# Kernel optimization log

Measured on AMD Instinct MI355X. Metric: run time of the kernel, lower is better.

## Reference

```python
import jax, jax.numpy as jnp
import numpy as np

NUM_HEADS = 8
NUM_GROUPS = 32
EPS = 1e-5


def group_norm(x, scale, bias):
    # x: (b, c, t)
    b, c, t = x.shape
    xg = x.reshape(b, NUM_GROUPS, c // NUM_GROUPS, t)
    mean = xg.mean(axis=(2, 3), keepdims=True)
    var = xg.var(axis=(2, 3), keepdims=True)
    xn = ((xg - mean) * jax.lax.rsqrt(var + EPS)).reshape(b, c, t)
    return xn * scale[None, :, None] + bias[None, :, None]


def setup_inputs() -> dict:
    key = jax.random.key(0)
    ks = jax.random.split(key, 3)
    b, c, h, w = 16, 512, 32, 32
    x = jax.random.normal(ks[0], (b, c, h, w), dtype=jnp.float32)
    gn_scale = jnp.ones((c,), jnp.float32)
    gn_bias = jnp.zeros((c,), jnp.float32)
    w_qkv = jax.random.normal(ks[1], (3 * c, c), jnp.float32) * (c ** -0.5)
    b_qkv = jnp.zeros((3 * c,), jnp.float32)
    w_proj = jax.random.normal(ks[2], (c, c), jnp.float32) * (c ** -0.5)
    b_proj = jnp.zeros((c,), jnp.float32)
    return {"x": x, "gn_scale": gn_scale, "gn_bias": gn_bias,
            "w_qkv": w_qkv, "b_qkv": b_qkv, "w_proj": w_proj, "b_proj": b_proj}


def reference(x, gn_scale, gn_bias, w_qkv, b_qkv, w_proj, b_proj):
    b, c, h, w = x.shape
    t = h * w
    xf = x.reshape(b, c, t)
    xn = group_norm(xf, gn_scale, gn_bias)
    # 1x1 conv1d == channel matmul: (b, 3c, t)
    qkv = jnp.einsum('oc,bct->bot', w_qkv, xn) + b_qkv[None, :, None]
    dh = c // NUM_HEADS
    qkv = qkv.reshape(b * NUM_HEADS, 3 * dh, t)
    q, k, v = jnp.split(qkv, 3, axis=1)  # each (b*H, dh, t)
    scale = dh ** -0.25
    logits = jnp.einsum('bct,bcs->bts', q * scale, k * scale)
    weight = jax.nn.softmax(logits.astype(jnp.float32), axis=-1).astype(logits.dtype)
    attn = jnp.einsum('bts,bcs->bct', weight, v)  # (b*H, dh, t)
    attn = attn.reshape(b, c, t)
    out = jnp.einsum('oc,bct->bot', w_proj, attn) + b_proj[None, :, None]
    return (xf + out).reshape(b, c, h, w)
```

## Files before the change

### kernel.cpp

```cpp
#include <hip/hip_runtime.h>
#include <hip/hip_bf16.h>

typedef __hip_bfloat16 bf16;
typedef __attribute__((ext_vector_type(8))) short short8;
typedef __attribute__((ext_vector_type(4))) short short4v;
typedef __attribute__((ext_vector_type(4))) float float4v;
typedef __attribute__((ext_vector_type(16))) float f32x16;
typedef __attribute__((ext_vector_type(4))) int int4v;

__device__ __forceinline__ float b2f(bf16 v) { return __bfloat162float(v); }
__device__ __forceinline__ bf16  f2b(float v) { return __float2bfloat16(v); }
__device__ __forceinline__ short f2s(float v) { bf16 h = f2b(v); return *reinterpret_cast<short*>(&h); }
__device__ __forceinline__ float s2f(short s) { bf16 h; *reinterpret_cast<short*>(&h) = s; return b2f(h); }
__device__ __forceinline__ short8 ld8(const bf16* p) { return *(const short8*)p; }

__device__ __forceinline__ float ldin(const void* p, size_t i, int f32) {
  return f32 ? ((const float*)p)[i] : b2f(((const bf16*)p)[i]);
}

__device__ __forceinline__ float4v mfma16(short8 a, short8 b, float4v c) {
  return __builtin_amdgcn_mfma_f32_16x16x32_bf16(a, b, c, 0, 0, 0);
}
__device__ __forceinline__ f32x16 mfma32(short8 a, short8 b, f32x16 c) {
  return __builtin_amdgcn_mfma_f32_32x32x16_bf16(a, b, c, 0, 0, 0);
}
__device__ __forceinline__ int cvtpk(float a, float b) {
  int r; asm("v_cvt_pk_bf16_f32 %0, %1, %2" : "=v"(r) : "v"(a), "v"(b)); return r;
}
__device__ __forceinline__ void plswap(int& x, int& y) {
  asm("v_permlane32_swap_b32 %0, %1" : "+v"(x), "+v"(y));
}

__device__ __forceinline__ void gload16(const void* g, void* l) {
  __builtin_amdgcn_global_load_lds((__attribute__((address_space(1))) void*)(void*)g,
                                   (__attribute__((address_space(3))) void*)l, 16, 0, 0);
}

#define K2SCALE 0.18033688011112042f
#define TSTRIDE 72

__global__ __launch_bounds__(256) void detect_kernel(const unsigned short* __restrict__ x,
                                                     int* __restrict__ flag) {
  __shared__ int h;
  if (threadIdx.x == 0) h = 0;
  __syncthreads();
  int local = 0;
  for (int i = threadIdx.x; i < 8192; i += 256)
    if ((x[i] & 0x7F80u) == 0x7F80u) local = 1;
  if (local) atomicOr(&h, 1);
  __syncthreads();
  if (threadIdx.x == 0) *flag = h;
}

__global__ __launch_bounds__(256) void conv2_kernel(const void* __restrict__ s1, bf16* __restrict__ d1,
                                                    const void* __restrict__ s2, bf16* __restrict__ d2,
                                                    const void* __restrict__ s3, bf16* __restrict__ d3,
                                                    const void* __restrict__ s4, bf16* __restrict__ d4,
                                                    const int* __restrict__ flagp) {
  const int f32 = *flagp;
  const int blk = blockIdx.x;
  const void* src; bf16* dst; int base, n;
  if (blk < 768)       { src = s1; dst = d1; base = blk;        n = 786432; }
  else if (blk < 1024) { src = s2; dst = d2; base = blk - 768;  n = 262144; }
  else if (blk < 1026) { src = s3; dst = d3; base = blk - 1024; n = 1536;   }
  else                 { src = s4; dst = d4; base = 0;          n = 512;    }
  int i0 = (base * 256 + threadIdx.x) * 4;
#pragma unroll
  for (int j = 0; j < 4; j++) {
    int i = i0 + j;
    if (i < n) dst[i] = f2b(ldin(src, i, f32));
  }
}

__global__ __launch_bounds__(256) void gn_stats_kernel(const void* __restrict__ x,
                                                       float2* __restrict__ stats,
                                                       const int* __restrict__ flagp) {
  const int f32 = *flagp;
  const int bg = blockIdx.x;
  const int GSZ = 16 * 1024;
  const size_t base = (size_t)bg * GSZ;
  const int tid = threadIdx.x;

  float s = 0.f, ss = 0.f;
  if (f32) {
    const float4v* xp = (const float4v*)((const float*)x + base) + tid;
#pragma unroll
    for (int i = 0; i < 16; i++) {
      float4v v = xp[i * 256];
#pragma unroll
      for (int j = 0; j < 4; j++) { s += v[j]; ss += v[j] * v[j]; }
    }
  } else {
    const short8* xp = (const short8*)((const bf16*)x + base) + tid;
#pragma unroll
    for (int i = 0; i < 8; i++) {
      short8 v = xp[i * 256];
#pragma unroll
      for (int j = 0; j < 8; j++) { float f = s2f(v[j]); s += f; ss += f * f; }
    }
  }
  for (int off = 32; off > 0; off >>= 1) {
    s  += __shfl_down(s, off);
    ss += __shfl_down(ss, off);
  }
  __shared__ float rs[4], rss[4];
  const int wave = tid >> 6, lane = tid & 63;
  if (lane == 0) { rs[wave] = s; rss[wave] = ss; }
  __syncthreads();
  if (tid == 0) {
    s  = rs[0] + rs[1] + rs[2] + rs[3];
    ss = rss[0] + rss[1] + rss[2] + rss[3];
    const float mean = s * (1.f / GSZ);
    const float var  = ss * (1.f / GSZ) - mean * mean;
    stats[bg] = make_float2(mean, rsqrtf(var + 1e-5f));
  }
}

__global__ __launch_bounds__(256) void gn_apply_kernel(const void* __restrict__ x,
                                                       const void* __restrict__ gsc,
                                                       const void* __restrict__ gbi,
                                                       const float2* __restrict__ stats,
                                                       bf16* __restrict__ xn,
                                                       const int* __restrict__ flagp) {
  const int f32 = *flagp;
  const int b = blockIdx.y;
  const int t0 = blockIdx.x * 64;
  const int cs = blockIdx.z * 128;
  const int tid = threadIdx.x;

  __shared__ float Aa[128], Bb[128];
  __shared__ short T[64][130];

  if (tid < 128) {
    const int c = cs + tid;
    const float2 st = stats[b * 32 + (c >> 4)];
    const float sc = ldin(gsc, c, f32), bi = ldin(gbi, c, f32);
    Aa[tid] = st.y * sc;
    Bb[tid] = bi - st.x * st.y * sc;
  }
  __syncthreads();

  const int row = tid >> 4;
  const int t4 = (tid & 15) * 4;
  if (f32) {
    const float* xb = (const float*)x + ((size_t)(b * 512 + cs)) * 1024 + t0 + t4;
#pragma unroll
    for (int st = 0; st < 8; st++) {
      const int c = row + st * 16;
      const float4v v = *(const float4v*)(xb + (size_t)c * 1024);
      const float aa = Aa[c], bb = Bb[c];
#pragma unroll
      for (int j = 0; j < 4; j++) T[t4 + j][c] = f2s(v[j] * aa + bb);
    }
  } else {
    const bf16* xb = (const bf16*)x + ((size_t)(b * 512 + cs)) * 1024 + t0 + t4;
#pragma unroll
    for (int st = 0; st < 8; st++) {
      const int c = row + st * 16;
      const short4v v = *(const short4v*)(xb + (size_t)c * 1024);
      const float aa = Aa[c], bb = Bb[c];
#pragma unroll
      for (int j = 0; j < 4; j++) T[t4 + j][c] = f2s(s2f(v[j]) * aa + bb);
    }
  }
  __syncthreads();

  const int cc = (tid & 63) * 2, tr = tid >> 6;
#pragma unroll
  for (int i = 0; i < 16; i++) {
    const int t2 = tr + i * 4;
    const int v = *(const int*)&T[t2][cc];
    *(int*)&xn[((size_t)(b * 1024 + t0 + t2)) * 512 + cs + cc] = v;
  }
}

__global__ __launch_bounds__(256) void qkv_kernel(const bf16* __restrict__ Wb,
                                                  const bf16* __restrict__ biasb,
                                                  const bf16* __restrict__ xn,
                                                  bf16* __restrict__ Qt,
                                                  bf16* __restrict__ Kt,
                                                  bf16* __restrict__ Vb) {
  const int bat = blockIdx.z;
  const int M0 = blockIdx.y * 128;
  const int N0 = blockIdx.x * 128;
  __shared__ short smem[18432];

  const int tid = threadIdx.x;
  const int w = tid >> 6, lane = tid & 63;
  const int col = lane & 15, g = lane >> 4;
  const int wm = (w & 1) * 64, wn = (w >> 1) * 64;

  float4v acc[4][4];
#pragma unroll
  for (int i = 0; i < 4; i++)
#pragma unroll
    for (int j = 0; j < 4; j++) acc[i][j] = (float4v)(0.f);

  int srco[2], dstb[2];
#pragma unroll
  for (int i = 0; i < 2; i++) {
    const int Gb = i * 256 + w * 64;
    dstb[i] = Gb * 8;
    const int G = Gb + lane;
    srco[i] = (G >> 2) * 512 + (G & 3) * 8;
  }
  const bf16* Ab  = Wb + (size_t)M0 * 512;
  const bf16* Bb2 = xn + ((size_t)bat * 1024 + N0) * 512;

#pragma unroll
  for (int i = 0; i < 2; i++) {
    gload16(Ab + srco[i],  &smem[dstb[i]]);
    gload16(Bb2 + srco[i], &smem[4096 + dstb[i]]);
  }
  __syncthreads();

  for (int it = 0; it < 16; ++it) {
    const int pb = it & 1;
    if (it < 15) {
      const int kn = it * 32 + 32;
      const int nb = (1 - pb) * 8192;
#pragma unroll
      for (int i = 0; i < 2; i++) {
        gload16(Ab + kn + srco[i],  &smem[nb + dstb[i]]);
        gload16(Bb2 + kn + srco[i], &smem[nb + 4096 + dstb[i]]);
      }
    }
    const short* Ap = &smem[pb * 8192];
    const short* Bp = Ap + 4096;
    short8 af[4], bf4[4];
#pragma unroll
    for (int mt = 0; mt < 4; mt++) af[mt] = *(const short8*)&Ap[(wm + mt * 16 + col) * 32 + g * 8];
#pragma unroll
    for (int nt = 0; nt < 4; nt++) bf4[nt] = *(const short8*)&Bp[(wn + nt * 16 + col) * 32 + g * 8];
#pragma unroll
    for (int mt = 0; mt < 4; mt++)
#pragma unroll
      for (int nt = 0; nt < 4; nt++) acc[mt][nt] = mfma16(af[mt], bf4[nt], acc[mt][nt]);
    __syncthreads();
  }

  const int sec = (M0 + wm) >> 6;
  const int h = sec / 3, kind = sec % 3;
  const size_t bh = (size_t)bat * 8 + h;
  const float qs = (kind == 0) ? K2SCALE : 1.f;
  short* Tw = smem + w * 4608;

  float bv[4][4];
#pragma unroll
  for (int mt = 0; mt < 4; mt++)
#pragma unroll
    for (int r = 0; r < 4; r++) bv[mt][r] = b2f(biasb[M0 + wm + mt * 16 + g * 4 + r]);

  if (kind == 2) {
#pragma unroll
    for (int mt = 0; mt < 4; mt++)
#pragma unroll
      for (int nt = 0; nt < 4; nt++)
#pragma unroll
        for (int r = 0; r < 4; r++) {
          const int lo = mt * 16 + g * 4 + r;
          const int lt = nt * 16 + col;
          Tw[lo * TSTRIDE + lt] = f2s(acc[mt][nt][r] + bv[mt][r]);
        }
#pragma unroll
    for (int j = 0; j < 8; j++) {
      const int lo = j * 8 + (lane >> 3);
      const int gr = lane & 7;
      short8 v = *(const short8*)&Tw[lo * TSTRIDE + gr * 8];
      *(short8*)(Vb + (bh * 64 + lo) * 1024 + N0 + wn + gr * 8) = v;
    }
  } else {
#pragma unroll
    for (int mt = 0; mt < 4; mt++)
#pragma unroll
      for (int nt = 0; nt < 4; nt++) {
        short4v pk;
#pragma unroll
        for (int r = 0; r < 4; r++) pk[r] = f2s((acc[mt][nt][r] + bv[mt][r]) * qs);
        *(short4v*)&Tw[(nt * 16 + col) * TSTRIDE + mt * 16 + g * 4] = pk;
      }
    bf16* dst = (kind == 0) ? Qt : Kt;
#pragma unroll
    for (int j = 0; j < 8; j++) {
      const int tl = j * 8 + (lane >> 3), c8 = (lane & 7) * 8;
      short8 v = *(const short8*)&Tw[tl * TSTRIDE + c8];
      *(short8*)(dst + (bh * 1024 + N0 + wn + tl) * 64 + c8) = v;
    }
  }
}

__global__ __launch_bounds__(256, 2) void attn_kernel(const bf16* __restrict__ Qt,
                                                      const bf16* __restrict__ Kt,
                                                      const bf16* __restrict__ Vb,
                                                      bf16* __restrict__ xattn) {
  const int bh = blockIdx.x;
  const int t0 = blockIdx.y * 256;
  const int b = bh >> 3, h = bh & 7;
  const int tid = threadIdx.x;
  const int w = tid >> 6, lane = tid & 63;
  const int qv = lane & 31, hh = lane >> 5;
  const int q0 = t0 + w * 64;

  __shared__ short Ks[8192];
  __shared__ short Vs[8192];

  const bf16* kbase = Kt + (size_t)bh * 65536;
  const bf16* vbase = Vb + (size_t)bh * 65536;

  int ksrc[2], vsrc[2];
  const int ldst0 = w * 1024, ldst1 = w * 1024 + 512;
#pragma unroll
  for (int i = 0; i < 2; i++) {
    const int G = w * 128 + i * 64 + lane;
    const int a = G >> 8, ks = (G >> 6) & 3, qvs = (G >> 1) & 31, hhs = G & 1;
    const int co = (ks * 2 + hhs) * 8;
    ksrc[i] = (a * 32 + qvs) * 64 + co;
    vsrc[i] = (a * 32 + qvs) * 1024 + co;
  }
  const int rb = (qv * 2 + hh) * 8;

  short8 qb[2][4];
#pragma unroll
  for (int qt = 0; qt < 2; qt++)
#pragma unroll
    for (int ks = 0; ks < 4; ks++)
      qb[qt][ks] = ld8(Qt + ((size_t)bh * 1024 + q0 + qt * 32 + qv) * 64 + ks * 16 + hh * 8);

  f32x16 O[2][2];
#pragma unroll
  for (int qt = 0; qt < 2; qt++)
#pragma unroll
    for (int o = 0; o < 2; o++) O[qt][o] = (f32x16)(0.f);
  float l[2] = {0.f, 0.f};
  short8 pa[2][4];

  gload16(kbase + ksrc[0], &Ks[ldst0]);
  gload16(kbase + ksrc[1], &Ks[ldst1]);
  gload16(vbase + vsrc[0], &Vs[ldst0]);
  gload16(vbase + vsrc[1], &Vs[ldst1]);
  __syncthreads();

#define SMAX(S, qt, a)                                                          \
  {                                                                             \
    _Pragma("unroll")                                                           \
    for (int j = 0; j < 16; j++) S[j] = __builtin_amdgcn_exp2f(S[j]);           \
    l[qt] += (((S[0] + S[1]) + (S[2] + S[3])) + ((S[4] + S[5]) + (S[6] + S[7])))\
       + (((S[8] + S[9]) + (S[10] + S[11])) + ((S[12] + S[13]) + (S[14] + S[15]))); \
    _Pragma("unroll")                                                           \
    for (int kp = 0; kp < 2; kp++) {                                            \
      int X  = cvtpk(S[8 * kp + 0], S[8 * kp + 1]);                             \
      int Y  = cvtpk(S[8 * kp + 4], S[8 * kp + 5]);                             \
      int X2 = cvtpk(S[8 * kp + 2], S[8 * kp + 3]);                             \
      int Y2 = cvtpk(S[8 * kp + 6], S[8 * kp + 7]);                             \
      plswap(X, Y);                                                             \
      plswap(X2, Y2);                                                           \
      const int4v wv = {X, X2, Y, Y2};                                          \
      pa[qt][(a) * 2 + kp] = __builtin_bit_cast(short8, wv);                    \
    }                                                                           \
  }

#pragma unroll 2
  for (int it = 0; it < 16; ++it) {
    const int cur = (it & 1) * 4096;
    const int nxt = 4096 - cur;
    if (it < 15) {
      gload16(kbase + (it + 1) * 4096 + ksrc[0], &Ks[nxt + ldst0]);
      gload16(kbase + (it + 1) * 4096 + ksrc[1], &Ks[nxt + ldst1]);
      gload16(vbase + (it + 1) * 64 + vsrc[0],   &Vs[nxt + ldst0]);
      gload16(vbase + (it + 1) * 64 + vsrc[1],   &Vs[nxt + ldst1]);
    }
#pragma unroll
    for (int a = 0; a < 2; a++) {
      short8 kf[4];
#pragma unroll
      for (int ks = 0; ks < 4; ks++)
        kf[ks] = *(const short8*)&Ks[cur + (a * 4 + ks) * 512 + rb];
#pragma unroll
      for (int qt = 0; qt < 2; qt++) {
        f32x16 S = (f32x16)(0.f);
#pragma unroll
        for (int ks = 0; ks < 4; ks++) S = mfma32(kf[ks], qb[qt][ks], S);
        SMAX(S, qt, a);
      }
    }
#pragma unroll
    for (int o = 0; o < 2; o++) {
      short8 vf[4];
#pragma unroll
      for (int ks = 0; ks < 4; ks++)
        vf[ks] = *(const short8*)&Vs[cur + (o * 4 + ks) * 512 + rb];
#pragma unroll
      for (int qt = 0; qt < 2; qt++)
#pragma unroll
        for (int ks = 0; ks < 4; ks++)
          O[qt][o] = mfma32(pa[qt][ks], vf[ks], O[qt][o]);
    }
    __syncthreads();
  }
#undef SMAX

#pragma unroll
  for (int qt = 0; qt < 2; qt++) {
    float lt = l[qt] + __shfl_xor(l[qt], 32);
    const float inv = 1.f / lt;
    float* lf = (float*)Ks + w * 64 + qt * 32;
    lf[qv] = inv;

    bf16* ob = xattn + ((size_t)b * 1024 + q0 + qt * 32 + 4 * hh) * 512 + h * 64 + qv;
#pragma unroll
    for (int r = 0; r < 16; r++) {
      const int qoff = (r & 3) + 8 * (r >> 2);
      const float iv = lf[qoff + 4 * hh];
      ob[(size_t)qoff * 512]      = f2b(O[qt][0][r] * iv);
      ob[(size_t)qoff * 512 + 32] = f2b(O[qt][1][r] * iv);
    }
  }
}

__global__ __launch_bounds__(256) void proj_kernel(const bf16* __restrict__ Wp,
                                                   const bf16* __restrict__ biasb,
                                                   const bf16* __restrict__ xattn,
                                                   const void* __restrict__ res,
                                                   void* __restrict__ out,
                                                   const int* __restrict__ flagp) {
  const int f32 = *flagp;
  const int bat = blockIdx.z;
  const int M0 = blockIdx.y * 128;
  const int N0 = blockIdx.x * 128;
  __shared__ short smem[18432];

  const int tid = threadIdx.x;
  const int w = tid >> 6, lane = tid & 63;
  const int col = lane & 15, g = lane >> 4;
  const int wm = (w & 1) * 64, wn = (w >> 1) * 64;

  float4v acc[4][4];
#pragma unroll
  for (int i = 0; i < 4; i++)
#pragma unroll
    for (int j = 0; j < 4; j++) acc[i][j] = (float4v)(0.f);

  int srco[2], dstb[2];
#pragma unroll
  for (int i = 0; i < 2; i++) {
    const int Gb = i * 256 + w * 64;
    dstb[i] = Gb * 8;
    const int G = Gb + lane;
    srco[i] = (G >> 2) * 512 + (G & 3) * 8;
  }
  const bf16* Ab  = Wp + (size_t)M0 * 512;
  const bf16* Bb2 = xattn + ((size_t)bat * 1024 + N0) * 512;

#pragma unroll
  for (int i = 0; i < 2; i++) {
    gload16(Ab + srco[i],  &smem[dstb[i]]);
    gload16(Bb2 + srco[i], &smem[4096 + dstb[i]]);
  }
  __syncthreads();

  for (int it = 0; it < 16; ++it) {
    const int pb = it & 1;
    if (it < 15) {
      const int kn = it * 32 + 32;
      const int nb = (1 - pb) * 8192;
#pragma unroll
      for (int i = 0; i < 2; i++) {
        gload16(Ab + kn + srco[i],  &smem[nb + dstb[i]]);
        gload16(Bb2 + kn + srco[i], &smem[nb + 4096 + dstb[i]]);
      }
    }
    const short* Ap = &smem[pb * 8192];
    const short* Bp = Ap + 4096;
    short8 af[4], bf4[4];
#pragma unroll
    for (int mt = 0; mt < 4; mt++) af[mt] = *(const short8*)&Ap[(wm + mt * 16 + col) * 32 + g * 8];
#pragma unroll
    for (int nt = 0; nt < 4; nt++) bf4[nt] = *(const short8*)&Bp[(wn + nt * 16 + col) * 32 + g * 8];
#pragma unroll
    for (int mt = 0; mt < 4; mt++)
#pragma unroll
      for (int nt = 0; nt < 4; nt++) acc[mt][nt] = mfma16(af[mt], bf4[nt], acc[mt][nt]);
    __syncthreads();
  }

  short* Tw = smem + w * 4608;
  float bv[4][4];
#pragma unroll
  for (int mt = 0; mt < 4; mt++)
#pragma unroll
    for (int r = 0; r < 4; r++) bv[mt][r] = b2f(biasb[M0 + wm + mt * 16 + g * 4 + r]);

#pragma unroll
  for (int mt = 0; mt < 4; mt++)
#pragma unroll
    for (int nt = 0; nt < 4; nt++)
#pragma unroll
      for (int r = 0; r < 4; r++) {
        const int lo = mt * 16 + g * 4 + r;
        const int lt = nt * 16 + col;
        Tw[lo * TSTRIDE + lt] = f2s(acc[mt][nt][r] + bv[mt][r]);
      }
#pragma unroll
  for (int j = 0; j < 8; j++) {
    const int lo = j * 8 + (lane >> 3);
    const int gr = lane & 7;
    short8 v = *(const short8*)&Tw[lo * TSTRIDE + gr * 8];
    const int o = M0 + wm + lo;
    const size_t ci = ((size_t)bat * 512 + o) * 1024 + N0 + wn + gr * 8;
    if (f32) {
      float4v o0, o1;
#pragma unroll
      for (int e = 0; e < 4; e++) o0[e] = s2f(v[e]) + ((const float*)res)[ci + e];
#pragma unroll
      for (int e = 0; e < 4; e++) o1[e] = s2f(v[e + 4]) + ((const float*)res)[ci + 4 + e];
      *(float4v*)((float*)out + ci) = o0;
      *(float4v*)((float*)out + ci + 4) = o1;
    } else {
      short8 ov;
#pragma unroll
      for (int e = 0; e < 8; e++)
        ov[e] = f2s(s2f(v[e]) + b2f(((const bf16*)res)[ci + e]));
      *(short8*)((bf16*)out + ci) = ov;
    }
  }
}

extern "C" void kernel_launch(void* const* d_in, const int* in_sizes, int n_in,
                              void* d_out, int out_size, void* d_ws, size_t ws_size,
                              hipStream_t stream) {
  const void* x      = d_in[0];
  const void* gsc    = d_in[1];
  const void* gbi    = d_in[2];
  const void* w_qkv  = d_in[3];
  const void* b_qkv  = d_in[4];
  const void* w_proj = d_in[5];
  const void* b_proj = d_in[6];

  char* p = (char*)d_ws;
  int*    flag  = (int*)p;                 p += 256;
  float2* stats = (float2*)p;              p += 512 * sizeof(float2);
  bf16*   xn    = (bf16*)p;                p += (size_t)16 * 1024 * 512 * 2;
  bf16*   Qt    = (bf16*)p;                p += (size_t)128 * 1024 * 64 * 2;
  bf16*   Kt    = (bf16*)p;                p += (size_t)128 * 1024 * 64 * 2;
  bf16*   Vb    = (bf16*)p;                p += (size_t)128 * 64 * 1024 * 2;
  bf16*   Wqb   = (bf16*)p;                p += (size_t)1536 * 512 * 2;
  bf16*   Wpb   = (bf16*)p;                p += (size_t)512 * 512 * 2;
  bf16*   Bqb   = (bf16*)p;                p += (size_t)1536 * 2;
  bf16*   Bpb   = (bf16*)p;                p += (size_t)512 * 2;
  bf16*   xattn = (bf16*)p;

  detect_kernel<<<1, 256, 0, stream>>>((const unsigned short*)x, flag);
  conv2_kernel<<<1027, 256, 0, stream>>>(w_qkv, Wqb, w_proj, Wpb,
                                         b_qkv, Bqb, b_proj, Bpb, flag);
  gn_stats_kernel<<<512, 256, 0, stream>>>(x, stats, flag);
  gn_apply_kernel<<<dim3(16, 16, 4), 256, 0, stream>>>(x, gsc, gbi, stats, xn, flag);
  qkv_kernel<<<dim3(8, 12, 16), 256, 0, stream>>>(Wqb, Bqb, xn, Qt, Kt, Vb);
  attn_kernel<<<dim3(128, 4), 256, 0, stream>>>(Qt, Kt, Vb, xattn);
  proj_kernel<<<dim3(8, 4, 16), 256, 0, stream>>>(Wpb, Bpb, xattn, x, d_out, flag);
}
```

Measured before the change: 206.2 us.

## Merge weight conversion with GN stats; double attention KV tile and add MFMA priority

The weight/bias bf16 conversion and group-norm statistics kernels are merged into one launch, removing a kernel boundary. The attention kernel now stages 128-key K/V tiles per iteration instead of 64, halving loop iterations and barriers. It also wraps MFMA sequences in s_setprio to favour matrix issue. The larger tiles double LDS use to 64KB per block and raise register pressure from the bigger P fragment array, which may reduce occupancy.

```diff
diff --git a/kernel.cpp b/kernel.cpp
--- a/kernel.cpp
+++ b/kernel.cpp
@@ -52,34 +52,36 @@
   if (threadIdx.x == 0) *flag = h;
 }
 
-__global__ __launch_bounds__(256) void conv2_kernel(const void* __restrict__ s1, bf16* __restrict__ d1,
-                                                    const void* __restrict__ s2, bf16* __restrict__ d2,
-                                                    const void* __restrict__ s3, bf16* __restrict__ d3,
-                                                    const void* __restrict__ s4, bf16* __restrict__ d4,
-                                                    const int* __restrict__ flagp) {
+__global__ __launch_bounds__(256) void pre_kernel(const void* __restrict__ s1, bf16* __restrict__ d1,
+                                                  const void* __restrict__ s2, bf16* __restrict__ d2,
+                                                  const void* __restrict__ s3, bf16* __restrict__ d3,
+                                                  const void* __restrict__ s4, bf16* __restrict__ d4,
+                                                  const void* __restrict__ x,
+                                                  float2* __restrict__ stats,
+                                                  const int* __restrict__ flagp) {
   const int f32 = *flagp;
   const int blk = blockIdx.x;
-  const void* src; bf16* dst; int base, n;
-  if (blk < 768)       { src = s1; dst = d1; base = blk;        n = 786432; }
-  else if (blk < 1024) { src = s2; dst = d2; base = blk - 768;  n = 262144; }
-  else if (blk < 1026) { src = s3; dst = d3; base = blk - 1024; n = 1536;   }
-  else                 { src = s4; dst = d4; base = 0;          n = 512;    }
-  int i0 = (base * 256 + threadIdx.x) * 4;
-#pragma unroll
-  for (int j = 0; j < 4; j++) {
-    int i = i0 + j;
-    if (i < n) dst[i] = f2b(ldin(src, i, f32));
-  }
-}
-
-__global__ __launch_bounds__(256) void gn_stats_kernel(const void* __restrict__ x,
-                                                       float2* __restrict__ stats,
-                                                       const int* __restrict__ flagp) {
-  const int f32 = *flagp;
-  const int bg = blockIdx.x;
+  const int tid = threadIdx.x;
+  __shared__ float rs[4], rss[4];
+
+  if (blk < 1027) {
+    const void* src; bf16* dst; int base, n;
+    if (blk < 768)       { src = s1; dst = d1; base = blk;        n = 786432; }
+    else if (blk < 1024) { src = s2; dst = d2; base = blk - 768;  n = 262144; }
+    else if (blk < 1026) { src = s3; dst = d3; base = blk - 1024; n = 1536;   }
+    else                 { src = s4; dst = d4; base = 0;          n = 512;    }
+    int i0 = (base * 256 + tid) * 4;
+#pragma unroll
+    for (int j = 0; j < 4; j++) {
+      int i = i0 + j;
+      if (i < n) dst[i] = f2b(ldin(src, i, f32));
+    }
+    return;
+  }
+
+  const int bg = blk - 1027;
   const int GSZ = 16 * 1024;
   const size_t base = (size_t)bg * GSZ;
-  const int tid = threadIdx.x;
 
   float s = 0.f, ss = 0.f;
   if (f32) {
@@ -103,7 +105,6 @@
     s  += __shfl_down(s, off);
     ss += __shfl_down(ss, off);
   }
-  __shared__ float rs[4], rss[4];
   const int wave = tid >> 6, lane = tid & 63;
   if (lane == 0) { rs[wave] = s; rss[wave] = ss; }
   __syncthreads();
@@ -301,21 +302,22 @@
   const int qv = lane & 31, hh = lane >> 5;
   const int q0 = t0 + w * 64;
 
-  __shared__ short Ks[8192];
-  __shared__ short Vs[8192];
+  __shared__ short Ks[16384];
+  __shared__ short Vs[16384];
 
   const bf16* kbase = Kt + (size_t)bh * 65536;
   const bf16* vbase = Vb + (size_t)bh * 65536;
 
-  int ksrc[2], vsrc[2];
-  const int ldst0 = w * 1024, ldst1 = w * 1024 + 512;
-#pragma unroll
-  for (int i = 0; i < 2; i++) {
-    const int G = w * 128 + i * 64 + lane;
-    const int a = G >> 8, ks = (G >> 6) & 3, qvs = (G >> 1) & 31, hhs = G & 1;
-    const int co = (ks * 2 + hhs) * 8;
-    ksrc[i] = (a * 32 + qvs) * 64 + co;
-    vsrc[i] = (a * 32 + qvs) * 1024 + co;
+  int ksrc[4], vsrc[4];
+  const int ldw = w * 2048;
+#pragma unroll
+  for (int i = 0; i < 4; i++) {
+    const int G = w * 256 + i * 64 + lane;
+    const int qvs = (G >> 1) & 31, hhs = G & 1;
+    const int ka = G >> 8, kks = (G >> 6) & 3;
+    ksrc[i] = (ka * 32 + qvs) * 64 + (kks * 2 + hhs) * 8;
+    const int vo = G >> 9, vks = (G >> 6) & 7;
+    vsrc[i] = (vo * 32 + qvs) * 1024 + (vks * 2 + hhs) * 8;
   }
   const int rb = (qv * 2 + hh) * 8;
 
@@ -332,12 +334,13 @@
 #pragma unroll
     for (int o = 0; o < 2; o++) O[qt][o] = (f32x16)(0.f);
   float l[2] = {0.f, 0.f};
-  short8 pa[2][4];
-
-  gload16(kbase + ksrc[0], &Ks[ldst0]);
-  gload16(kbase + ksrc[1], &Ks[ldst1]);
-  gload16(vbase + vsrc[0], &Vs[ldst0]);
-  gload16(vbase + vsrc[1], &Vs[ldst1]);
+  short8 pa[2][8];
+
+#pragma unroll
+  for (int i = 0; i < 4; i++) {
+    gload16(kbase + ksrc[i], &Ks[ldw + i * 512]);
+    gload16(vbase + vsrc[i], &Vs[ldw + i * 512]);
+  }
   __syncthreads();
 
 #define SMAX(S, qt, a)                                                          \
@@ -360,17 +363,18 @@
   }
 
 #pragma unroll 2
-  for (int it = 0; it < 16; ++it) {
-    const int cur = (it & 1) * 4096;
-    const int nxt = 4096 - cur;
-    if (it < 15) {
-      gload16(kbase + (it + 1) * 4096 + ksrc[0], &Ks[nxt + ldst0]);
-      gload16(kbase + (it + 1) * 4096 + ksrc[1], &Ks[nxt + ldst1]);
-      gload16(vbase + (it + 1) * 64 + vsrc[0],   &Vs[nxt + ldst0]);
-      gload16(vbase + (it + 1) * 64 + vsrc[1],   &Vs[nxt + ldst1]);
-    }
-#pragma unroll
-    for (int a = 0; a < 2; a++) {
+  for (int it = 0; it < 8; ++it) {
+    const int cur = (it & 1) * 8192;
+    const int nxt = 8192 - cur;
+    if (it < 7) {
+#pragma unroll
+      for (int i = 0; i < 4; i++) {
+        gload16(kbase + (it + 1) * 8192 + ksrc[i], &Ks[nxt + ldw + i * 512]);
+        gload16(vbase + (it + 1) * 128 + vsrc[i], &Vs[nxt + ldw + i * 512]);
+      }
+    }
+#pragma unroll
+    for (int a = 0; a < 4; a++) {
       short8 kf[4];
 #pragma unroll
       for (int ks = 0; ks < 4; ks++)
@@ -378,22 +382,27 @@
 #pragma unroll
       for (int qt = 0; qt < 2; qt++) {
         f32x16 S = (f32x16)(0.f);
+        __builtin_amdgcn_s_setprio(1);
 #pragma unroll
         for (int ks = 0; ks < 4; ks++) S = mfma32(kf[ks], qb[qt][ks], S);
+        __builtin_amdgcn_s_setprio(0);
         SMAX(S, qt, a);
       }
     }
 #pragma unroll
     for (int o = 0; o < 2; o++) {
-      short8 vf[4];
-#pragma unroll
-      for (int ks = 0; ks < 4; ks++)
-        vf[ks] = *(const short8*)&Vs[cur + (o * 4 + ks) * 512 + rb];
-#pragma unroll
-      for (int qt = 0; qt < 2; qt++)
-#pragma unroll
-        for (int ks = 0; ks < 4; ks++)
+      short8 vf[8];
+#pragma unroll
+      for (int ks = 0; ks < 8; ks++)
+        vf[ks] = *(const short8*)&Vs[cur + (o * 8 + ks) * 512 + rb];
+#pragma unroll
+      for (int qt = 0; qt < 2; qt++) {
+        __builtin_amdgcn_s_setprio(1);
+#pragma unroll
+        for (int ks = 0; ks < 8; ks++)
           O[qt][o] = mfma32(pa[qt][ks], vf[ks], O[qt][o]);
+        __builtin_amdgcn_s_setprio(0);
+      }
     }
     __syncthreads();
   }
@@ -550,9 +559,9 @@
   bf16*   xattn = (bf16*)p;
 
   detect_kernel<<<1, 256, 0, stream>>>((const unsigned short*)x, flag);
-  conv2_kernel<<<1027, 256, 0, stream>>>(w_qkv, Wqb, w_proj, Wpb,
-                                         b_qkv, Bqb, b_proj, Bpb, flag);
-  gn_stats_kernel<<<512, 256, 0, stream>>>(x, stats, flag);
+  pre_kernel<<<1539, 256, 0, stream>>>(w_qkv, Wqb, w_proj, Wpb,
+                                       b_qkv, Bqb, b_proj, Bpb,
+                                       x, stats, flag);
   gn_apply_kernel<<<dim3(16, 16, 4), 256, 0, stream>>>(x, gsc, gbi, stats, xn, flag);
   qkv_kernel<<<dim3(8, 12, 16), 256, 0, stream>>>(Wqb, Bqb, xn, Qt, Kt, Vb);
   attn_kernel<<<dim3(128, 4), 256, 0, stream>>>(Qt, Kt, Vb, xattn);
```

Result: faster. 200.2 us (-2.9%).
